# Kernel tuning notes

Hardware: AMD Instinct MI355X
Metric: run time of the kernel (lower is better)

Reference implementation:

```python
import jax, jax.numpy as jnp
import numpy as np

N, E, F_IN, H, G = 100000, 3200000, 128, 256, 64


def gcn_layer(x, src, dst, W, b, n):
    # GCNConv with added self-loops and symmetric normalization:
    # out = D^{-1/2} (A + I) D^{-1/2} X W + b
    h = x @ W  # [n, H]
    deg = jax.ops.segment_sum(jnp.ones_like(dst, dtype=h.dtype), dst, num_segments=n) + 1.0
    dinv = jax.lax.rsqrt(deg)
    coef = dinv[src] * dinv[dst]  # [E]
    agg = jax.ops.segment_sum(h[src] * coef[:, None], dst, num_segments=n)
    out = agg + h * (dinv * dinv)[:, None]  # self-loop term: 1/deg
    return out + b


def global_mean_pool(x, batch, num_graphs):
    sums = jax.ops.segment_sum(x, batch, num_segments=num_graphs)
    cnts = jax.ops.segment_sum(jnp.ones((x.shape[0],), x.dtype), batch, num_segments=num_graphs)
    return sums / jnp.maximum(cnts, 1.0)[:, None]


def conv_pass(x, edge_index, batch, params):
    (W0, b0, W1, b1, W2, b2, lin0_W, lin0_b) = params
    src, dst = edge_index[0], edge_index[1]
    n = x.shape[0]
    x = jax.nn.relu(gcn_layer(x, src, dst, W0, b0, n))
    x = jax.nn.relu(gcn_layer(x, src, dst, W1, b1, n))
    x = gcn_layer(x, src, dst, W2, b2, n)
    x = global_mean_pool(x, batch, G)
    # dropout(p=0.5) is identity in eval mode
    return x @ lin0_W + lin0_b  # [G, H/2]


def setup_inputs() -> dict:
    key = jax.random.key(0)
    ks = jax.random.split(key, 20)
    d = {}
    for i, nm in enumerate(['x0', 'x1', 'x2']):
        d[nm] = jax.random.normal(ks[i], (N, F_IN), dtype=jnp.float32)
    for i, nm in enumerate(['edge_index0', 'edge_index1', 'edge_index2']):
        d[nm] = jax.random.randint(ks[3 + i], (2, E), 0, N, dtype=jnp.int32)
    for i, nm in enumerate(['batch0', 'batch1', 'batch2']):
        d[nm] = jnp.sort(jax.random.randint(ks[6 + i], (N,), 0, G, dtype=jnp.int32))
    s = lambda fan: 1.0 / np.sqrt(fan)
    d['W0'] = jax.random.uniform(ks[9], (F_IN, H), jnp.float32, -s(F_IN), s(F_IN))
    d['b0'] = jnp.zeros((H,), jnp.float32)
    d['W1'] = jax.random.uniform(ks[10], (H, H), jnp.float32, -s(H), s(H))
    d['b1'] = jnp.zeros((H,), jnp.float32)
    d['W2'] = jax.random.uniform(ks[11], (H, H), jnp.float32, -s(H), s(H))
    d['b2'] = jnp.zeros((H,), jnp.float32)
    d['lin0_W'] = jax.random.uniform(ks[12], (H, H // 2), jnp.float32, -s(H), s(H))
    d['lin0_b'] = jax.random.uniform(ks[13], (H // 2,), jnp.float32, -s(H), s(H))
    d['lin_W'] = jax.random.uniform(ks[14], (H, 1), jnp.float32, -s(H), s(H))
    d['lin_b'] = jax.random.uniform(ks[15], (1,), jnp.float32, -s(H), s(H))
    return d


def reference(x0, x1, x2, edge_index0, edge_index1, edge_index2,
              batch0, batch1, batch2,
              W0, b0, W1, b1, W2, b2, lin0_W, lin0_b, lin_W, lin_b):
    params = (W0, b0, W1, b1, W2, b2, lin0_W, lin0_b)
    z0 = conv_pass(x0, edge_index0, batch0, params)
    z1 = conv_pass(x1, edge_index1, batch1, params)
    z2 = conv_pass(x2, edge_index2, batch2, params)
    EPS = 1e-6  # torch F.pairwise_distance eps
    dist_p = jnp.linalg.norm(z0 - z1 + EPS, axis=1)
    dist_n = jnp.linalg.norm(z0 - z2 + EPS, axis=1)
    y1 = jnp.concatenate([z0, z1], axis=1) @ lin_W + lin_b
    y2 = jnp.concatenate([z0, z2], axis=1) @ lin_W + lin_b
    score_p = jax.nn.sigmoid(y1)
    score_n = jax.nn.sigmoid(y2)
    correct = jnp.sum(dist_n - dist_p > 0).astype(jnp.int32).reshape(1)
    correct_score = jnp.sum(score_p - score_n > 0).astype(jnp.int32).reshape(1)
    return (z0, z1, z2, correct, score_p, score_n, correct_score)
```

## Files before the change

### kernel.cpp

```cpp
#include <hip/hip_runtime.h>
#include <math.h>

#define NN 100000
#define EE 3200000

typedef __attribute__((ext_vector_type(8))) short bf16x8;
typedef __attribute__((ext_vector_type(4))) float f32x4;

__device__ __forceinline__ unsigned short f2b(float f) {
  unsigned u = __float_as_uint(f);
  u += 0x7fffu + ((u >> 16) & 1u);
  return (unsigned short)(u >> 16);
}
__device__ __forceinline__ float b2f(unsigned short s) {
  return __uint_as_float(((unsigned)s) << 16);
}
__device__ __forceinline__ float blo(unsigned u) { return __uint_as_float(u << 16); }
__device__ __forceinline__ float bhi(unsigned u) { return __uint_as_float(u & 0xffff0000u); }
__device__ __forceinline__ unsigned pack2(float lo, float hi) {
  return ((unsigned)f2b(hi) << 16) | (unsigned)f2b(lo);
}

#define WPB 8192
#define NODES_PER_PASS 16384
#define NPASS 7
#define HB 64

__global__ void zero_int(int* __restrict__ p, int n) {
  int i = blockIdx.x * 256 + threadIdx.x;
  if (i < n) p[i] = 0;
}

__global__ __launch_bounds__(256) void hist_part(
    const int* __restrict__ d0, const int* __restrict__ d1, const int* __restrict__ d2,
    unsigned* __restrict__ partials) {
  __shared__ unsigned cnt[WPB];
  int b = blockIdx.x, p = blockIdx.y, g = blockIdx.z;
  const int* dst = (g == 0) ? d0 : (g == 1) ? d1 : d2;
  for (int i = threadIdx.x; i < WPB; i += 256) cnt[i] = 0;
  __syncthreads();
  unsigned lo = (unsigned)(p * NODES_PER_PASS);
  int base = b * (EE / HB);
  int end = base + EE / HB;
  for (int i = base + threadIdx.x * 4; i < end; i += 256 * 4) {
    int4 d = *(const int4*)(dst + i);
    unsigned n0 = (unsigned)d.x - lo;
    unsigned n1 = (unsigned)d.y - lo;
    unsigned n2 = (unsigned)d.z - lo;
    unsigned n3 = (unsigned)d.w - lo;
    if (n0 < NODES_PER_PASS) atomicAdd(&cnt[n0 >> 1], 1u << ((n0 & 1) * 16));
    if (n1 < NODES_PER_PASS) atomicAdd(&cnt[n1 >> 1], 1u << ((n1 & 1) * 16));
    if (n2 < NODES_PER_PASS) atomicAdd(&cnt[n2 >> 1], 1u << ((n2 & 1) * 16));
    if (n3 < NODES_PER_PASS) atomicAdd(&cnt[n3 >> 1], 1u << ((n3 & 1) * 16));
  }
  __syncthreads();
  unsigned* out = partials + ((size_t)((g * NPASS + p) * HB + b)) * WPB;
  for (int i = threadIdx.x; i < WPB; i += 256) out[i] = cnt[i];
}

__global__ void hist_reduce(const unsigned* __restrict__ partials,
                            unsigned* __restrict__ deg3w) {
  int i = blockIdx.x * 256 + threadIdx.x;
  int p = blockIdx.y, g = blockIdx.z;
  unsigned s = 0;
  const unsigned* base = partials + ((size_t)((g * NPASS + p) * HB)) * WPB + i;
#pragma unroll 16
  for (int b = 0; b < HB; ++b) s += base[(size_t)b * WPB];
  int word = p * WPB + i;
  if (word < NN / 2) deg3w[(size_t)g * (NN / 2) + word] = s;
}

__global__ void calc_dinv3(const unsigned short* __restrict__ deg3u,
                           float* __restrict__ dinv3, int n3) {
  int i = blockIdx.x * 256 + threadIdx.x;
  if (i < n3) dinv3[i] = 1.0f / sqrtf((float)(deg3u[i] + 1));
}

#define SCHUNK 1024
#define NCHUNK 98

__global__ __launch_bounds__(256) void scan_part(const unsigned short* __restrict__ deg3u,
                                                 int* __restrict__ bsum) {
  int c = blockIdx.x, g = blockIdx.y;
  const unsigned short* deg = deg3u + (size_t)g * NN;
  int base = c * SCHUNK;
  int s = 0;
  for (int i = threadIdx.x; i < SCHUNK; i += 256) {
    int idx = base + i;
    s += (idx < NN) ? (int)deg[idx] : 0;
  }
#pragma unroll
  for (int o = 32; o; o >>= 1) s += __shfl_down(s, o, 64);
  __shared__ int ws[4];
  if ((threadIdx.x & 63) == 0) ws[threadIdx.x >> 6] = s;
  __syncthreads();
  if (threadIdx.x == 0) bsum[g * NCHUNK + c] = ws[0] + ws[1] + ws[2] + ws[3];
}

__global__ __launch_bounds__(128) void scan_mid(int* __restrict__ bsum) {
  int g = blockIdx.x;
  int t = threadIdx.x;
  int v = (t < NCHUNK) ? bsum[g * NCHUNK + t] : 0;
  int lane = t & 63, wv = t >> 6;
  int x = v;
#pragma unroll
  for (int o = 1; o < 64; o <<= 1) {
    int tt = __shfl_up(x, o, 64);
    if (lane >= o) x += tt;
  }
  __shared__ int w0sum;
  if (wv == 0 && lane == 63) w0sum = x;
  __syncthreads();
  int excl = x - v + (wv ? w0sum : 0);
  if (t < NCHUNK) bsum[g * NCHUNK + t] = excl;
}

__global__ __launch_bounds__(1024) void scan_final(const unsigned short* __restrict__ deg3u,
    const int* __restrict__ bsum, int* __restrict__ offs3) {
  int c = blockIdx.x, g = blockIdx.y;
  const unsigned short* deg = deg3u + (size_t)g * NN;
  int* offs = offs3 + (size_t)g * (NN + 1);
  int t = threadIdx.x;
  int idx = c * SCHUNK + t;
  int v = (idx < NN) ? (int)deg[idx] : 0;
  int lane = t & 63, wv = t >> 6;
  int x = v;
#pragma unroll
  for (int o = 1; o < 64; o <<= 1) {
    int tt = __shfl_up(x, o, 64);
    if (lane >= o) x += tt;
  }
  __shared__ int ws[16];
  if (lane == 63) ws[wv] = x;
  __syncthreads();
  int woff = 0;
  for (int j = 0; j < wv; ++j) woff += ws[j];
  if (idx < NN) offs[idx] = bsum[g * NCHUNK + c] + woff + x - v;
  if (idx == NN - 1) offs[NN] = EE;
}

__global__ void fill_csr(const int* __restrict__ src, const int* __restrict__ dst,
                         const float* __restrict__ dinv, const int* __restrict__ offs,
                         int* __restrict__ fillc, unsigned long long* __restrict__ ent,
                         int e) {
  int i = blockIdx.x * 256 + threadIdx.x;
  if (i >= e) return;
  int d = dst[i], s = src[i];
  int pos = offs[d] + atomicAdd(&fillc[d], 1);
  unsigned long long w = (unsigned long long)(unsigned)__float_as_int(dinv[s]);
  ent[pos] = (w << 32) | (unsigned)s;
}

__global__ void conv_bf(const float* __restrict__ in, unsigned* __restrict__ out, int n4) {
  int i = blockIdx.x * 256 + threadIdx.x;
  if (i >= n4) return;
  float4 v = ((const float4*)in)[i];
  ((uint2*)out)[i] = make_uint2(pack2(v.x, v.y), pack2(v.z, v.w));
}

__global__ void conv_wt(const float* __restrict__ W, unsigned short* __restrict__ Wt, int K) {
  int i = blockIdx.x * 256 + threadIdx.x;
  if (i >= 256 * K) return;
  int nn = i / K, kk = i - nn * K;
  Wt[i] = f2b(W[(size_t)kk * 256 + nn]);
}

__global__ __launch_bounds__(256) void agg256_bf(const unsigned short* __restrict__ x,
    const unsigned long long* __restrict__ ent, const int* __restrict__ offs,
    const float* __restrict__ dinv, unsigned short* __restrict__ y, int n) {
  int v = (blockIdx.x * 256 + threadIdx.x) >> 6;
  v = __builtin_amdgcn_readfirstlane(v);
  int lane = threadIdx.x & 63;
  if (v >= n) return;
  float dv = dinv[v];
  const uint2* selfp = (const uint2*)(x + ((size_t)(unsigned)v << 8)) + lane;
  uint2 self = *selfp;
  float a0 = dv * blo(self.x), a1 = dv * bhi(self.x);
  float a2 = dv * blo(self.y), a3 = dv * bhi(self.y);
  int s = offs[v], e = offs[v + 1];
  int i = s;
  for (; i + 3 < e; i += 4) {
    unsigned long long p0 = ent[i], p1 = ent[i + 1], p2 = ent[i + 2], p3 = ent[i + 3];
    unsigned s0 = (unsigned)p0, s1 = (unsigned)p1, s2 = (unsigned)p2, s3 = (unsigned)p3;
    float w0 = __uint_as_float((unsigned)(p0 >> 32));
    float w1 = __uint_as_float((unsigned)(p1 >> 32));
    float w2 = __uint_as_float((unsigned)(p2 >> 32));
    float w3 = __uint_as_float((unsigned)(p3 >> 32));
    uint2 r0 = *((const uint2*)(x + ((size_t)s0 << 8)) + lane);
    uint2 r1 = *((const uint2*)(x + ((size_t)s1 << 8)) + lane);
    uint2 r2 = *((const uint2*)(x + ((size_t)s2 << 8)) + lane);
    uint2 r3 = *((const uint2*)(x + ((size_t)s3 << 8)) + lane);
    a0 += w0 * blo(r0.x); a1 += w0 * bhi(r0.x); a2 += w0 * blo(r0.y); a3 += w0 * bhi(r0.y);
    a0 += w1 * blo(r1.x); a1 += w1 * bhi(r1.x); a2 += w1 * blo(r1.y); a3 += w1 * bhi(r1.y);
    a0 += w2 * blo(r2.x); a1 += w2 * bhi(r2.x); a2 += w2 * blo(r2.y); a3 += w2 * bhi(r2.y);
    a0 += w3 * blo(r3.x); a1 += w3 * bhi(r3.x); a2 += w3 * blo(r3.y); a3 += w3 * bhi(r3.y);
  }
  for (; i < e; ++i) {
    unsigned long long p0 = ent[i];
    unsigned s0 = (unsigned)p0;
    float w0 = __uint_as_float((unsigned)(p0 >> 32));
    uint2 r0 = *((const uint2*)(x + ((size_t)s0 << 8)) + lane);
    a0 += w0 * blo(r0.x); a1 += w0 * bhi(r0.x); a2 += w0 * blo(r0.y); a3 += w0 * bhi(r0.y);
  }
  uint2* yp = (uint2*)(y + ((size_t)(unsigned)v << 8)) + lane;
  *yp = make_uint2(pack2(dv * a0, dv * a1), pack2(dv * a2, dv * a3));
}

__global__ __launch_bounds__(256) void agg128_bf(const unsigned short* __restrict__ x,
    const unsigned long long* __restrict__ ent, const int* __restrict__ offs,
    const float* __restrict__ dinv, unsigned short* __restrict__ y, int n) {
  int v = (blockIdx.x * 256 + threadIdx.x) >> 6;
  v = __builtin_amdgcn_readfirstlane(v);
  int lane = threadIdx.x & 63;
  if (v >= n) return;
  float dv = dinv[v];
  const unsigned* selfp = (const unsigned*)(x + ((size_t)(unsigned)v << 7)) + lane;
  unsigned self = *selfp;
  float a0 = dv * blo(self), a1 = dv * bhi(self);
  int s = offs[v], e = offs[v + 1];
  int i = s;
  for (; i + 3 < e; i += 4) {
    unsigned long long p0 = ent[i], p1 = ent[i + 1], p2 = ent[i + 2], p3 = ent[i + 3];
    unsigned s0 = (unsigned)p0, s1 = (unsigned)p1, s2 = (unsigned)p2, s3 = (unsigned)p3;
    float w0 = __uint_as_float((unsigned)(p0 >> 32));
    float w1 = __uint_as_float((unsigned)(p1 >> 32));
    float w2 = __uint_as_float((unsigned)(p2 >> 32));
    float w3 = __uint_as_float((unsigned)(p3 >> 32));
    unsigned r0 = *((const unsigned*)(x + ((size_t)s0 << 7)) + lane);
    unsigned r1 = *((const unsigned*)(x + ((size_t)s1 << 7)) + lane);
    unsigned r2 = *((const unsigned*)(x + ((size_t)s2 << 7)) + lane);
    unsigned r3 = *((const unsigned*)(x + ((size_t)s3 << 7)) + lane);
    a0 += w0 * blo(r0); a1 += w0 * bhi(r0);
    a0 += w1 * blo(r1); a1 += w1 * bhi(r1);
    a0 += w2 * blo(r2); a1 += w2 * bhi(r2);
    a0 += w3 * blo(r3); a1 += w3 * bhi(r3);
  }
  for (; i < e; ++i) {
    unsigned long long p0 = ent[i];
    unsigned s0 = (unsigned)p0;
    float w0 = __uint_as_float((unsigned)(p0 >> 32));
    unsigned r0 = *((const unsigned*)(x + ((size_t)s0 << 7)) + lane);
    a0 += w0 * blo(r0); a1 += w0 * bhi(r0);
  }
  unsigned* yp = (unsigned*)(y + ((size_t)(unsigned)v << 7)) + lane;
  *yp = pack2(dv * a0, dv * a1);
}

#define LDA 40
__global__ __launch_bounds__(256) void gemm_mfma(
    const unsigned short* __restrict__ A, const unsigned short* __restrict__ Bt,
    const float* __restrict__ bias, unsigned short* __restrict__ C,
    int M, int K, int do_relu) {
  __shared__ unsigned short As[128 * LDA];
  __shared__ unsigned short Bs[128 * LDA];
  int tid = threadIdx.x;
  int row0 = blockIdx.x * 128;
  int col0 = blockIdx.y * 128;
  int wave = tid >> 6, lane = tid & 63;
  int wm = wave >> 1, wn = wave & 1;
  int lr = lane & 15, quad = lane >> 4;

  f32x4 acc[4][4];
#pragma unroll
  for (int i = 0; i < 4; ++i)
#pragma unroll
    for (int j = 0; j < 4; ++j) acc[i][j] = (f32x4){0.f, 0.f, 0.f, 0.f};

  for (int k0 = 0; k0 < K; k0 += 32) {
#pragma unroll
    for (int p = 0; p < 2; ++p) {
      int i = tid + p * 256;
      int r = i >> 2, q = i & 3;
      int row = row0 + r; if (row >= M) row = M - 1;
      uint4 va = *(const uint4*)(A + (size_t)row * K + k0 + q * 8);
      *(uint4*)&As[r * LDA + q * 8] = va;
      uint4 vb = *(const uint4*)(Bt + (size_t)(col0 + r) * K + k0 + q * 8);
      *(uint4*)&Bs[r * LDA + q * 8] = vb;
    }
    __syncthreads();
    bf16x8 af[4], bf[4];
#pragma unroll
    for (int mi = 0; mi < 4; ++mi)
      af[mi] = *(const bf16x8*)&As[(wm * 64 + mi * 16 + lr) * LDA + quad * 8];
#pragma unroll
    for (int ni = 0; ni < 4; ++ni)
      bf[ni] = *(const bf16x8*)&Bs[(wn * 64 + ni * 16 + lr) * LDA + quad * 8];
#pragma unroll
    for (int mi = 0; mi < 4; ++mi)
#pragma unroll
      for (int ni = 0; ni < 4; ++ni)
        acc[mi][ni] = __builtin_amdgcn_mfma_f32_16x16x32_bf16(af[mi], bf[ni], acc[mi][ni], 0, 0, 0);
    __syncthreads();
  }

  float bv[4];
#pragma unroll
  for (int ni = 0; ni < 4; ++ni) bv[ni] = bias[col0 + wn * 64 + ni * 16 + lr];
#pragma unroll
  for (int mi = 0; mi < 4; ++mi) {
#pragma unroll
    for (int r = 0; r < 4; ++r) {
      int grow = row0 + wm * 64 + mi * 16 + quad * 4 + r;
      if (grow < M) {
#pragma unroll
        for (int ni = 0; ni < 4; ++ni) {
          float v = acc[mi][ni][r] + bv[ni];
          if (do_relu) v = fmaxf(v, 0.f);
          C[(size_t)grow * 256 + col0 + wn * 64 + ni * 16 + lr] = f2b(v);
        }
      }
    }
  }
}

__global__ __launch_bounds__(256) void pool_sum_bf(const unsigned short* __restrict__ h,
    const int* __restrict__ batch, float* __restrict__ sums,
    float* __restrict__ cnts, int n) {
  int f = threadIdx.x;
  int v0 = blockIdx.x * 128;
  if (v0 >= n) return;
  int vend = min(v0 + 128, n);
  int cur = batch[v0];
  float acc = 0.f;
  int cnt = 0;
  for (int v = v0; v < vend; ++v) {
    int b = batch[v];
    if (b != cur) {
      atomicAdd(&sums[cur * 256 + f], acc);
      if (f == 0) atomicAdd(&cnts[cur], (float)cnt);
      acc = 0.f; cnt = 0; cur = b;
    }
    acc += b2f(h[(size_t)v * 256 + f]);
    cnt++;
  }
  atomicAdd(&sums[cur * 256 + f], acc);
  if (f == 0) atomicAdd(&cnts[cur], (float)cnt);
}

__global__ __launch_bounds__(128) void pool_lin(const float* __restrict__ sums,
    const float* __restrict__ cnts, const float* __restrict__ W128,
    const float* __restrict__ b128, float* __restrict__ z) {
  int g = blockIdx.x, f = threadIdx.x;
  float inv = 1.0f / fmaxf(cnts[g], 1.0f);
  float acc = 0.f;
  for (int k = 0; k < 256; ++k)
    acc += (sums[g * 256 + k] * inv) * W128[k * 128 + f];
  z[g * 128 + f] = acc + b128[f];
}

__global__ __launch_bounds__(64) void final_triplet(const float* __restrict__ z,
    const float* __restrict__ lin_W, const float* __restrict__ lin_b,
    float* __restrict__ out) {
  int g = threadIdx.x;
  const float* z0 = z;
  const float* z1 = z + 8192;
  const float* z2 = z + 16384;
  float dp = 0.f, dn = 0.f;
  float y1 = lin_b[0], y2 = lin_b[0];
  for (int f = 0; f < 128; ++f) {
    float a = z0[g * 128 + f], b = z1[g * 128 + f], c = z2[g * 128 + f];
    float d1 = a - b + 1e-6f, d2 = a - c + 1e-6f;
    dp += d1 * d1; dn += d2 * d2;
    float w0 = lin_W[f], w1 = lin_W[128 + f];
    y1 += a * w0 + b * w1;
    y2 += a * w0 + c * w1;
  }
  dp = sqrtf(dp); dn = sqrtf(dn);
  float sp = 1.f / (1.f + expf(-y1));
  float sn = 1.f / (1.f + expf(-y2));
  out[24577 + g] = sp;
  out[24641 + g] = sn;
  unsigned long long m1 = __ballot(dn - dp > 0.f);
  unsigned long long m2 = __ballot(sp - sn > 0.f);
  if (g == 0) {
    out[24576] = (float)__popcll(m1);
    out[24705] = (float)__popcll(m2);
  }
}

extern "C" void kernel_launch(void* const* d_in, const int* in_sizes, int n_in,
                              void* d_out, int out_size, void* d_ws, size_t ws_size,
                              hipStream_t stream) {
  const float* xin[3]  = {(const float*)d_in[0], (const float*)d_in[1], (const float*)d_in[2]};
  const int* ei[3]     = {(const int*)d_in[3], (const int*)d_in[4], (const int*)d_in[5]};
  const int* batch[3]  = {(const int*)d_in[6], (const int*)d_in[7], (const int*)d_in[8]};
  const float* W0 = (const float*)d_in[9],  *b0 = (const float*)d_in[10];
  const float* W1 = (const float*)d_in[11], *b1 = (const float*)d_in[12];
  const float* W2 = (const float*)d_in[13], *b2 = (const float*)d_in[14];
  const float* lin0W = (const float*)d_in[15], *lin0b = (const float*)d_in[16];
  const float* linW  = (const float*)d_in[17], *linb  = (const float*)d_in[18];
  float* out = (float*)d_out;

  unsigned short* ybf = (unsigned short*)d_ws;
  unsigned short* hbf = ybf + (size_t)NN * 256;
  unsigned short* xbf = hbf + (size_t)NN * 256;
  unsigned long long* ent = (unsigned long long*)(xbf + (size_t)NN * 128);
  unsigned short* Wt0 = (unsigned short*)(ent + EE);
  unsigned short* Wt1 = Wt0 + 256 * 128;
  unsigned short* Wt2 = Wt1 + 256 * 256;
  int* fillc3 = (int*)(Wt2 + 256 * 256);
  float* sums3 = (float*)(fillc3 + 3 * NN);
  float* cnts3 = sums3 + 3 * 64 * 256;
  int zero_elems = 3 * NN + 3 * 64 * 256 + 3 * 64;
  float* dinv3 = cnts3 + 3 * 64;
  int* offs3 = (int*)(dinv3 + 3 * NN);
  unsigned* deg3w = (unsigned*)(offs3 + 3 * (NN + 1));
  int* bsum = (int*)(deg3w + 3 * (NN / 2));
  unsigned* partials = (unsigned*)ybf;
  const unsigned short* deg3u = (const unsigned short*)deg3w;

  const int EB = (EE + 255) / 256;
  dim3 ggrid((NN + 127) / 128, 2);

  conv_wt<<<(256 * 128 + 255) / 256, 256, 0, stream>>>(W0, Wt0, 128);
  conv_wt<<<(256 * 256 + 255) / 256, 256, 0, stream>>>(W1, Wt1, 256);
  conv_wt<<<(256 * 256 + 255) / 256, 256, 0, stream>>>(W2, Wt2, 256);

  zero_int<<<(zero_elems + 255) / 256, 256, 0, stream>>>(fillc3, zero_elems);
  hist_part<<<dim3(HB, NPASS, 3), 256, 0, stream>>>(ei[0] + EE, ei[1] + EE, ei[2] + EE, partials);
  hist_reduce<<<dim3(WPB / 256, NPASS, 3), 256, 0, stream>>>(partials, deg3w);
  calc_dinv3<<<(3 * NN + 255) / 256, 256, 0, stream>>>(deg3u, dinv3, 3 * NN);
  scan_part<<<dim3(NCHUNK, 3), 256, 0, stream>>>(deg3u, bsum);
  scan_mid<<<3, 128, 0, stream>>>(bsum);
  scan_final<<<dim3(NCHUNK, 3), 1024, 0, stream>>>(deg3u, bsum, offs3);

  for (int g = 0; g < 3; ++g) {
    const int* src = ei[g];
    const int* dst = ei[g] + EE;
    const float* dinv = dinv3 + (size_t)g * NN;
    const int* offs = offs3 + (size_t)g * (NN + 1);

    fill_csr<<<EB, 256, 0, stream>>>(src, dst, dinv, offs, fillc3 + (size_t)g * NN, ent, EE);

    conv_bf<<<(NN * 128 / 4 + 255) / 256, 256, 0, stream>>>(xin[g], (unsigned*)xbf, NN * 128 / 4);

    agg128_bf<<<(NN + 3) / 4, 256, 0, stream>>>(xbf, ent, offs, dinv, ybf, NN);
    gemm_mfma<<<ggrid, 256, 0, stream>>>(ybf, Wt0, b0, hbf, NN, 128, 1);
    agg256_bf<<<(NN + 3) / 4, 256, 0, stream>>>(hbf, ent, offs, dinv, ybf, NN);
    gemm_mfma<<<ggrid, 256, 0, stream>>>(ybf, Wt1, b1, hbf, NN, 256, 1);
    agg256_bf<<<(NN + 3) / 4, 256, 0, stream>>>(hbf, ent, offs, dinv, ybf, NN);
    gemm_mfma<<<ggrid, 256, 0, stream>>>(ybf, Wt2, b2, hbf, NN, 256, 0);

    pool_sum_bf<<<(NN + 127) / 128, 256, 0, stream>>>(hbf, batch[g],
        sums3 + (size_t)g * 64 * 256, cnts3 + (size_t)g * 64, NN);
    pool_lin<<<64, 128, 0, stream>>>(sums3 + (size_t)g * 64 * 256, cnts3 + (size_t)g * 64,
        lin0W, lin0b, out + g * 8192);
  }

  final_triplet<<<1, 64, 0, stream>>>(out, linW, linb, out);
}
```

Baseline: 2.940 ms.

## Defer last GCN weight multiply past mean pool and shrink CSR entries to indices

New measurement: 2.823 ms. 4.0% less time.

```diff
diff --git a/kernel.cpp b/kernel.cpp
--- a/kernel.cpp
+++ b/kernel.cpp
@@ -140,15 +140,14 @@
 }
 
 __global__ void fill_csr(const int* __restrict__ src, const int* __restrict__ dst,
-                         const float* __restrict__ dinv, const int* __restrict__ offs,
-                         int* __restrict__ fillc, unsigned long long* __restrict__ ent,
+                         const int* __restrict__ offs,
+                         int* __restrict__ fillc, int* __restrict__ ent,
                          int e) {
   int i = blockIdx.x * 256 + threadIdx.x;
   if (i >= e) return;
   int d = dst[i], s = src[i];
   int pos = offs[d] + atomicAdd(&fillc[d], 1);
-  unsigned long long w = (unsigned long long)(unsigned)__float_as_int(dinv[s]);
-  ent[pos] = (w << 32) | (unsigned)s;
+  ent[pos] = s;
 }
 
 __global__ void conv_bf(const float* __restrict__ in, unsigned* __restrict__ out, int n4) {
@@ -166,7 +165,7 @@
 }
 
 __global__ __launch_bounds__(256) void agg256_bf(const unsigned short* __restrict__ x,
-    const unsigned long long* __restrict__ ent, const int* __restrict__ offs,
+    const int* __restrict__ ent, const int* __restrict__ offs,
     const float* __restrict__ dinv, unsigned short* __restrict__ y, int n) {
   int v = (blockIdx.x * 256 + threadIdx.x) >> 6;
   v = __builtin_amdgcn_readfirstlane(v);
@@ -179,35 +178,47 @@
   float a2 = dv * blo(self.y), a3 = dv * bhi(self.y);
   int s = offs[v], e = offs[v + 1];
   int i = s;
+#define ACC4(rr, ww) { \
+    a0 += ww * blo(rr.x); a1 += ww * bhi(rr.x); \
+    a2 += ww * blo(rr.y); a3 += ww * bhi(rr.y); }
+  for (; i + 7 < e; i += 8) {
+    int s0 = ent[i],     s1 = ent[i + 1], s2 = ent[i + 2], s3 = ent[i + 3];
+    int s4 = ent[i + 4], s5 = ent[i + 5], s6 = ent[i + 6], s7 = ent[i + 7];
+    float w0 = dinv[s0], w1 = dinv[s1], w2 = dinv[s2], w3 = dinv[s3];
+    float w4 = dinv[s4], w5 = dinv[s5], w6 = dinv[s6], w7 = dinv[s7];
+    uint2 r0 = *((const uint2*)(x + ((size_t)(unsigned)s0 << 8)) + lane);
+    uint2 r1 = *((const uint2*)(x + ((size_t)(unsigned)s1 << 8)) + lane);
+    uint2 r2 = *((const uint2*)(x + ((size_t)(unsigned)s2 << 8)) + lane);
+    uint2 r3 = *((const uint2*)(x + ((size_t)(unsigned)s3 << 8)) + lane);
+    uint2 r4 = *((const uint2*)(x + ((size_t)(unsigned)s4 << 8)) + lane);
+    uint2 r5 = *((const uint2*)(x + ((size_t)(unsigned)s5 << 8)) + lane);
+    uint2 r6 = *((const uint2*)(x + ((size_t)(unsigned)s6 << 8)) + lane);
+    uint2 r7 = *((const uint2*)(x + ((size_t)(unsigned)s7 << 8)) + lane);
+    ACC4(r0, w0); ACC4(r1, w1); ACC4(r2, w2); ACC4(r3, w3);
+    ACC4(r4, w4); ACC4(r5, w5); ACC4(r6, w6); ACC4(r7, w7);
+  }
   for (; i + 3 < e; i += 4) {
-    unsigned long long p0 = ent[i], p1 = ent[i + 1], p2 = ent[i + 2], p3 = ent[i + 3];
-    unsigned s0 = (unsigned)p0, s1 = (unsigned)p1, s2 = (unsigned)p2, s3 = (unsigned)p3;
-    float w0 = __uint_as_float((unsigned)(p0 >> 32));
-    float w1 = __uint_as_float((unsigned)(p1 >> 32));
-    float w2 = __uint_as_float((unsigned)(p2 >> 32));
-    float w3 = __uint_as_float((unsigned)(p3 >> 32));
-    uint2 r0 = *((const uint2*)(x + ((size_t)s0 << 8)) + lane);
-    uint2 r1 = *((const uint2*)(x + ((size_t)s1 << 8)) + lane);
-    uint2 r2 = *((const uint2*)(x + ((size_t)s2 << 8)) + lane);
-    uint2 r3 = *((const uint2*)(x + ((size_t)s3 << 8)) + lane);
-    a0 += w0 * blo(r0.x); a1 += w0 * bhi(r0.x); a2 += w0 * blo(r0.y); a3 += w0 * bhi(r0.y);
-    a0 += w1 * blo(r1.x); a1 += w1 * bhi(r1.x); a2 += w1 * blo(r1.y); a3 += w1 * bhi(r1.y);
-    a0 += w2 * blo(r2.x); a1 += w2 * bhi(r2.x); a2 += w2 * blo(r2.y); a3 += w2 * bhi(r2.y);
-    a0 += w3 * blo(r3.x); a1 += w3 * bhi(r3.x); a2 += w3 * blo(r3.y); a3 += w3 * bhi(r3.y);
+    int s0 = ent[i], s1 = ent[i + 1], s2 = ent[i + 2], s3 = ent[i + 3];
+    float w0 = dinv[s0], w1 = dinv[s1], w2 = dinv[s2], w3 = dinv[s3];
+    uint2 r0 = *((const uint2*)(x + ((size_t)(unsigned)s0 << 8)) + lane);
+    uint2 r1 = *((const uint2*)(x + ((size_t)(unsigned)s1 << 8)) + lane);
+    uint2 r2 = *((const uint2*)(x + ((size_t)(unsigned)s2 << 8)) + lane);
+    uint2 r3 = *((const uint2*)(x + ((size_t)(unsigned)s3 << 8)) + lane);
+    ACC4(r0, w0); ACC4(r1, w1); ACC4(r2, w2); ACC4(r3, w3);
   }
   for (; i < e; ++i) {
-    unsigned long long p0 = ent[i];
-    unsigned s0 = (unsigned)p0;
-    float w0 = __uint_as_float((unsigned)(p0 >> 32));
-    uint2 r0 = *((const uint2*)(x + ((size_t)s0 << 8)) + lane);
-    a0 += w0 * blo(r0.x); a1 += w0 * bhi(r0.x); a2 += w0 * blo(r0.y); a3 += w0 * bhi(r0.y);
-  }
+    int s0 = ent[i];
+    float w0 = dinv[s0];
+    uint2 r0 = *((const uint2*)(x + ((size_t)(unsigned)s0 << 8)) + lane);
+    ACC4(r0, w0);
+  }
+#undef ACC4
   uint2* yp = (uint2*)(y + ((size_t)(unsigned)v << 8)) + lane;
   *yp = make_uint2(pack2(dv * a0, dv * a1), pack2(dv * a2, dv * a3));
 }
 
 __global__ __launch_bounds__(256) void agg128_bf(const unsigned short* __restrict__ x,
-    const unsigned long long* __restrict__ ent, const int* __restrict__ offs,
+    const int* __restrict__ ent, const int* __restrict__ offs,
     const float* __restrict__ dinv, unsigned short* __restrict__ y, int n) {
   int v = (blockIdx.x * 256 + threadIdx.x) >> 6;
   v = __builtin_amdgcn_readfirstlane(v);
@@ -219,29 +230,39 @@
   float a0 = dv * blo(self), a1 = dv * bhi(self);
   int s = offs[v], e = offs[v + 1];
   int i = s;
+#define ACC2(rr, ww) { a0 += ww * blo(rr); a1 += ww * bhi(rr); }
+  for (; i + 7 < e; i += 8) {
+    int s0 = ent[i],     s1 = ent[i + 1], s2 = ent[i + 2], s3 = ent[i + 3];
+    int s4 = ent[i + 4], s5 = ent[i + 5], s6 = ent[i + 6], s7 = ent[i + 7];
+    float w0 = dinv[s0], w1 = dinv[s1], w2 = dinv[s2], w3 = dinv[s3];
+    float w4 = dinv[s4], w5 = dinv[s5], w6 = dinv[s6], w7 = dinv[s7];
+    unsigned r0 = *((const unsigned*)(x + ((size_t)(unsigned)s0 << 7)) + lane);
+    unsigned r1 = *((const unsigned*)(x + ((size_t)(unsigned)s1 << 7)) + lane);
+    unsigned r2 = *((const unsigned*)(x + ((size_t)(unsigned)s2 << 7)) + lane);
+    unsigned r3 = *((const unsigned*)(x + ((size_t)(unsigned)s3 << 7)) + lane);
+    unsigned r4 = *((const unsigned*)(x + ((size_t)(unsigned)s4 << 7)) + lane);
+    unsigned r5 = *((const unsigned*)(x + ((size_t)(unsigned)s5 << 7)) + lane);
+    unsigned r6 = *((const unsigned*)(x + ((size_t)(unsigned)s6 << 7)) + lane);
+    unsigned r7 = *((const unsigned*)(x + ((size_t)(unsigned)s7 << 7)) + lane);
+    ACC2(r0, w0); ACC2(r1, w1); ACC2(r2, w2); ACC2(r3, w3);
+    ACC2(r4, w4); ACC2(r5, w5); ACC2(r6, w6); ACC2(r7, w7);
+  }
   for (; i + 3 < e; i += 4) {
-    unsigned long long p0 = ent[i], p1 = ent[i + 1], p2 = ent[i + 2], p3 = ent[i + 3];
-    unsigned s0 = (unsigned)p0, s1 = (unsigned)p1, s2 = (unsigned)p2, s3 = (unsigned)p3;
-    float w0 = __uint_as_float((unsigned)(p0 >> 32));
-    float w1 = __uint_as_float((unsigned)(p1 >> 32));
-    float w2 = __uint_as_float((unsigned)(p2 >> 32));
-    float w3 = __uint_as_float((unsigned)(p3 >> 32));
-    unsigned r0 = *((const unsigned*)(x + ((size_t)s0 << 7)) + lane);
-    unsigned r1 = *((const unsigned*)(x + ((size_t)s1 << 7)) + lane);
-    unsigned r2 = *((const unsigned*)(x + ((size_t)s2 << 7)) + lane);
-    unsigned r3 = *((const unsigned*)(x + ((size_t)s3 << 7)) + lane);
-    a0 += w0 * blo(r0); a1 += w0 * bhi(r0);
-    a0 += w1 * blo(r1); a1 += w1 * bhi(r1);
-    a0 += w2 * blo(r2); a1 += w2 * bhi(r2);
-    a0 += w3 * blo(r3); a1 += w3 * bhi(r3);
+    int s0 = ent[i], s1 = ent[i + 1], s2 = ent[i + 2], s3 = ent[i + 3];
+    float w0 = dinv[s0], w1 = dinv[s1], w2 = dinv[s2], w3 = dinv[s3];
+    unsigned r0 = *((const unsigned*)(x + ((size_t)(unsigned)s0 << 7)) + lane);
+    unsigned r1 = *((const unsigned*)(x + ((size_t)(unsigned)s1 << 7)) + lane);
+    unsigned r2 = *((const unsigned*)(x + ((size_t)(unsigned)s2 << 7)) + lane);
+    unsigned r3 = *((const unsigned*)(x + ((size_t)(unsigned)s3 << 7)) + lane);
+    ACC2(r0, w0); ACC2(r1, w1); ACC2(r2, w2); ACC2(r3, w3);
   }
   for (; i < e; ++i) {
-    unsigned long long p0 = ent[i];
-    unsigned s0 = (unsigned)p0;
-    float w0 = __uint_as_float((unsigned)(p0 >> 32));
-    unsigned r0 = *((const unsigned*)(x + ((size_t)s0 << 7)) + lane);
-    a0 += w0 * blo(r0); a1 += w0 * bhi(r0);
-  }
+    int s0 = ent[i];
+    float w0 = dinv[s0];
+    unsigned r0 = *((const unsigned*)(x + ((size_t)(unsigned)s0 << 7)) + lane);
+    ACC2(r0, w0);
+  }
+#undef ACC2
   unsigned* yp = (unsigned*)(y + ((size_t)(unsigned)v << 7)) + lane;
   *yp = pack2(dv * a0, dv * a1);
 }
@@ -337,15 +358,24 @@
   if (f == 0) atomicAdd(&cnts[cur], (float)cnt);
 }
 
-__global__ __launch_bounds__(128) void pool_lin(const float* __restrict__ sums,
-    const float* __restrict__ cnts, const float* __restrict__ W128,
-    const float* __restrict__ b128, float* __restrict__ z) {
-  int g = blockIdx.x, f = threadIdx.x;
+__global__ __launch_bounds__(256) void pool_lin2(const float* __restrict__ sums,
+    const float* __restrict__ cnts, const float* __restrict__ W2,
+    const float* __restrict__ b2, const float* __restrict__ lin0W,
+    const float* __restrict__ lin0b, float* __restrict__ z) {
+  int g = blockIdx.x, t = threadIdx.x;
+  __shared__ float s[256], u[256];
   float inv = 1.0f / fmaxf(cnts[g], 1.0f);
-  float acc = 0.f;
-  for (int k = 0; k < 256; ++k)
-    acc += (sums[g * 256 + k] * inv) * W128[k * 128 + f];
-  z[g * 128 + f] = acc + b128[f];
+  s[t] = sums[g * 256 + t] * inv;
+  __syncthreads();
+  float acc = b2[t];
+  for (int j = 0; j < 256; ++j) acc += s[j] * W2[j * 256 + t];
+  u[t] = acc;
+  __syncthreads();
+  if (t < 128) {
+    float a2 = lin0b[t];
+    for (int k = 0; k < 256; ++k) a2 += u[k] * lin0W[k * 128 + t];
+    z[g * 128 + t] = a2;
+  }
 }
 
 __global__ __launch_bounds__(64) void final_triplet(const float* __restrict__ z,
@@ -394,11 +424,10 @@
   unsigned short* ybf = (unsigned short*)d_ws;
   unsigned short* hbf = ybf + (size_t)NN * 256;
   unsigned short* xbf = hbf + (size_t)NN * 256;
-  unsigned long long* ent = (unsigned long long*)(xbf + (size_t)NN * 128);
+  int* ent = (int*)(xbf + (size_t)NN * 128);
   unsigned short* Wt0 = (unsigned short*)(ent + EE);
   unsigned short* Wt1 = Wt0 + 256 * 128;
-  unsigned short* Wt2 = Wt1 + 256 * 256;
-  int* fillc3 = (int*)(Wt2 + 256 * 256);
+  int* fillc3 = (int*)(Wt1 + 256 * 256);
   float* sums3 = (float*)(fillc3 + 3 * NN);
   float* cnts3 = sums3 + 3 * 64 * 256;
   int zero_elems = 3 * NN + 3 * 64 * 256 + 3 * 64;
@@ -414,7 +443,6 @@
 
   conv_wt<<<(256 * 128 + 255) / 256, 256, 0, stream>>>(W0, Wt0, 128);
   conv_wt<<<(256 * 256 + 255) / 256, 256, 0, stream>>>(W1, Wt1, 256);
-  conv_wt<<<(256 * 256 + 255) / 256, 256, 0, stream>>>(W2, Wt2, 256);
 
   zero_int<<<(zero_elems + 255) / 256, 256, 0, stream>>>(fillc3, zero_elems);
   hist_part<<<dim3(HB, NPASS, 3), 256, 0, stream>>>(ei[0] + EE, ei[1] + EE, ei[2] + EE, partials);
@@ -430,7 +458,7 @@
     const float* dinv = dinv3 + (size_t)g * NN;
     const int* offs = offs3 + (size_t)g * (NN + 1);
 
-    fill_csr<<<EB, 256, 0, stream>>>(src, dst, dinv, offs, fillc3 + (size_t)g * NN, ent, EE);
+    fill_csr<<<EB, 256, 0, stream>>>(src, dst, offs, fillc3 + (size_t)g * NN, ent, EE);
 
     conv_bf<<<(NN * 128 / 4 + 255) / 256, 256, 0, stream>>>(xin[g], (unsigned*)xbf, NN * 128 / 4);
 
@@ -439,12 +467,11 @@
     agg256_bf<<<(NN + 3) / 4, 256, 0, stream>>>(hbf, ent, offs, dinv, ybf, NN);
     gemm_mfma<<<ggrid, 256, 0, stream>>>(ybf, Wt1, b1, hbf, NN, 256, 1);
     agg256_bf<<<(NN + 3) / 4, 256, 0, stream>>>(hbf, ent, offs, dinv, ybf, NN);
-    gemm_mfma<<<ggrid, 256, 0, stream>>>(ybf, Wt2, b2, hbf, NN, 256, 0);
-
-    pool_sum_bf<<<(NN + 127) / 128, 256, 0, stream>>>(hbf, batch[g],
+
+    pool_sum_bf<<<(NN + 127) / 128, 256, 0, stream>>>(ybf, batch[g],
         sums3 + (size_t)g * 64 * 256, cnts3 + (size_t)g * 64, NN);
-    pool_lin<<<64, 128, 0, stream>>>(sums3 + (size_t)g * 64 * 256, cnts3 + (size_t)g * 64,
-        lin0W, lin0b, out + g * 8192);
+    pool_lin2<<<64, 256, 0, stream>>>(sums3 + (size_t)g * 64 * 256, cnts3 + (size_t)g * 64,
+        W2, b2, lin0W, lin0b, out + g * 8192);
   }
 
   final_triplet<<<1, 64, 0, stream>>>(out, linW, linb, out);
```
